# Kernel optimization log

Measured on AMD Instinct MI355X. Metric: run time of the kernel, lower is better.

## Reference

```python
import jax, jax.numpy as jnp
import numpy as np

M, K, N = 4096, 4096, 12288
GS = 128                 # quantization group size
G = K // GS              # number of groups
PACK = 8                 # int4 values per int32


def _pack_nibbles(key, shape_packed, axis_len):
    # generate random int4 values and pack 8 per int32 (bit-faithful GPTQ layout)
    nib = jax.random.randint(key, shape_packed[:1] + (PACK,) + shape_packed[1:], 0, 16, dtype=jnp.uint32)
    shifts = (jnp.arange(PACK, dtype=jnp.uint32) * 4)[None, :, None]
    return jnp.sum(nib << shifts, axis=1).astype(jnp.int32)


def setup_inputs() -> dict:
    key = jax.random.key(0)
    k1, k2, k3, k4, k5 = jax.random.split(key, 5)
    x = jax.random.normal(k1, (M, K), dtype=jnp.float32) * 0.05
    qweight = _pack_nibbles(k2, (K // PACK, N), K)          # [K/8, N] int32
    qzeros = _pack_nibbles(k3, (G, N // PACK), N)           # [G, N/8] int32
    scales = jax.random.uniform(k4, (G, N), dtype=jnp.float32, minval=0.001, maxval=0.01)
    bias = jax.random.normal(k5, (N,), dtype=jnp.float32) * 0.01
    return {"x": x, "qweight": qweight, "qzeros": qzeros, "scales": scales, "bias": bias}


def _unpack_rows(q):
    # [R, C] int32 -> [R*8, C] int4 values unpacked along rows
    shifts = (jnp.arange(PACK, dtype=jnp.uint32) * 4)[None, :, None]
    nib = (q.astype(jnp.uint32)[:, None, :] >> shifts) & jnp.uint32(0xF)
    return nib.reshape(q.shape[0] * PACK, q.shape[1])


def _unpack_cols(q):
    # [R, C] int32 -> [R, C*8] int4 values unpacked along columns
    shifts = (jnp.arange(PACK, dtype=jnp.uint32) * 4)[None, None, :]
    nib = (q.astype(jnp.uint32)[:, :, None] >> shifts) & jnp.uint32(0xF)
    return nib.reshape(q.shape[0], q.shape[1] * PACK)


def reference(x, qweight, qzeros, scales, bias):
    # dequantize: w[k,n] = (q[k,n] - (z[g,n]+1)) * s[g,n],  g = k // GS
    q = _unpack_rows(qweight).astype(jnp.float32)                    # [K, N]
    z = (_unpack_cols(qzeros).astype(jnp.float32) + 1.0)             # [G, N]
    s = scales                                                       # [G, N]
    w = (q.reshape(G, GS, N) - z[:, None, :]) * s[:, None, :]        # [G, GS, N]
    w = w.reshape(K, N)
    return x @ w + bias
```

## Files before the change

### kernel.cpp

```cpp
#include <hip/hip_runtime.h>
#include <hip/hip_bf16.h>

namespace {
constexpr int Md = 4096, Kd = 4096, Nd = 12288;
constexpr int BM = 256, BN = 128, BK = 64;
constexpr int TK = Kd / BK;
constexpr int THREADS = 256;
constexpr size_t A_BYTES = (size_t)Md * Kd * 2;
constexpr int AS_T = BM * BK;
constexpr int BS_T = BN * BK;
constexpr int LDS_BYTES = (2 * AS_T + BS_T) * 2;

typedef __attribute__((ext_vector_type(4))) float f4;
typedef __attribute__((ext_vector_type(8))) _Float16 h8;
typedef __attribute__((ext_vector_type(2))) _Float16 h2;

constexpr unsigned M4  = 0x000F000Fu;
constexpr unsigned MAG = 0x64006400u;

__device__ __forceinline__ unsigned pkrtz(float lo, float hi) {
  return __builtin_bit_cast(unsigned, __builtin_amdgcn_cvt_pkrtz(lo, hi));
}

__global__ __launch_bounds__(256)
void cvtA_perm(const float* __restrict__ X, unsigned short* __restrict__ Xb, int n8) {
  int i = blockIdx.x * blockDim.x + threadIdx.x;
  const int stride = gridDim.x * blockDim.x;
  for (; i < n8; i += stride) {
    const f4* p = (const f4*)X + (size_t)i * 2;
    f4 a = p[0], b = p[1];
    uint4 o;
    o.x = pkrtz(a[0], b[0]); o.y = pkrtz(a[1], b[1]);
    o.z = pkrtz(a[2], b[2]); o.w = pkrtz(a[3], b[3]);
    ((uint4*)Xb)[i] = o;
  }
}

template<bool AWS>
__global__ __launch_bounds__(THREADS, 2)
void qgemm7(const float* __restrict__ X, const unsigned short* __restrict__ Xb,
            const int* __restrict__ QW, const int* __restrict__ QZ,
            const float* __restrict__ SC, const float* __restrict__ BS,
            float* __restrict__ OUT)
{
  extern __shared__ char smem[];
  unsigned short* As = (unsigned short*)smem;
  unsigned short* Bs = (unsigned short*)(smem + 2 * AS_T * 2);

  const int nwg = gridDim.x, cpx = nwg >> 3, b = blockIdx.x;
  const int swz = (b & 7) * cpx + (b >> 3);
  const int bm = swz / (Nd / BN), bn = swz % (Nd / BN);
  const int m0 = bm * BM, n0 = bn * BN;

  const int tid = threadIdx.x, lane = tid & 63, wid = tid >> 6;
  const int wr = wid >> 1, wc = wid & 1;

  const int n_l = tid & 127;
  const int k8b = (tid >> 7) * 4;
  const int nab = n0 + n_l;

  f4 acc[8][4];
  #pragma unroll
  for (int i = 0; i < 8; ++i)
    #pragma unroll
    for (int j = 0; j < 4; ++j) acc[i][j] = {0.0f, 0.0f, 0.0f, 0.0f};

  auto stageA = [&](int t, int buf) {
    #pragma unroll
    for (int i = 0; i < 8; ++i) {
      const int c = i * THREADS + tid;
      const int r = c >> 3, kbl = c & 7;
      const unsigned short* src = Xb + (size_t)(m0 + r) * Kd + t * BK + ((kbl ^ (r & 7)) << 3);
      __builtin_amdgcn_global_load_lds(
          (const __attribute__((address_space(1))) unsigned*)src,
          (__attribute__((address_space(3))) unsigned*)(As + buf * AS_T + c * 8),
          16, 0, 0);
    }
  };
  auto stageA_f = [&](int t, int buf) {
    #pragma unroll
    for (int i = 0; i < 8; ++i) {
      const int c = i * THREADS + tid;
      const int r = c >> 3, kbl = c & 7;
      const f4* src = (const f4*)(X + (size_t)(m0 + r) * Kd + t * BK + ((kbl ^ (r & 7)) << 3));
      f4 a = src[0], bb = src[1];
      uint4 o;
      o.x = pkrtz(a[0], bb[0]); o.y = pkrtz(a[1], bb[1]);
      o.z = pkrtz(a[2], bb[2]); o.w = pkrtz(a[3], bb[3]);
      *(uint4*)(As + buf * AS_T + c * 8) = o;
    }
  };

  auto loadB = [&](int t, int* w, unsigned& hs2, unsigned& hz2) {
    const int* qp = QW + (size_t)(t * 8 + k8b) * Nd + nab;
    #pragma unroll
    for (int i = 0; i < 4; ++i) w[i] = qp[(size_t)i * Nd];
    const int g = t >> 1;
    const float s = SC[(size_t)g * Nd + nab];
    const int z32 = QZ[(size_t)g * (Nd / 8) + (nab >> 3)];
    const int z = (z32 >> ((nab & 7) * 4)) & 15;
    const unsigned hz = 0x6400u + (unsigned)z + 1u;
    hz2 = hz * 0x10001u;
    const unsigned short hs = __builtin_bit_cast(unsigned short, (_Float16)s);
    hs2 = (unsigned)hs * 0x10001u;
  };
  auto writeB = [&](const int* w, unsigned hs2, unsigned hz2) {
    const h2 vz = __builtin_bit_cast(h2, hz2);
    const h2 vs = __builtin_bit_cast(h2, hs2);
    #pragma unroll
    for (int i = 0; i < 4; ++i) {
      const unsigned q = (unsigned)w[i];
      const int k8 = k8b + i;
      const unsigned p0 = (q & M4) | MAG;
      const unsigned p1 = ((q >> 4) & M4) | MAG;
      const unsigned p2 = ((q >> 8) & M4) | MAG;
      const unsigned p3 = ((q >> 12) & M4) | MAG;
      const h2 f0 = (__builtin_bit_cast(h2, p0) - vz) * vs;
      const h2 f1 = (__builtin_bit_cast(h2, p1) - vz) * vs;
      const h2 f2 = (__builtin_bit_cast(h2, p2) - vz) * vs;
      const h2 f3 = (__builtin_bit_cast(h2, p3) - vz) * vs;
      uint4 o;
      o.x = __builtin_bit_cast(unsigned, f0);
      o.y = __builtin_bit_cast(unsigned, f1);
      o.z = __builtin_bit_cast(unsigned, f2);
      o.w = __builtin_bit_cast(unsigned, f3);
      *(uint4*)(Bs + n_l * BK + ((k8 ^ (n_l & 7)) << 3)) = o;
    }
  };

  auto mfma_tile = [&](int cb) {
    const unsigned short* Ab = As + cb * AS_T;
    #pragma unroll
    for (int ks = 0; ks < 2; ++ks) {
      h8 af[8], bf[4];
      const int kb = ks * 4 + (lane >> 4);
      #pragma unroll
      for (int mi = 0; mi < 8; ++mi) {
        const int r = wr * 128 + mi * 16 + (lane & 15);
        af[mi] = *(const h8*)&Ab[r * BK + ((kb ^ (r & 7)) << 3)];
      }
      #pragma unroll
      for (int ni = 0; ni < 4; ++ni) {
        const int cc = wc * 64 + ni * 16 + (lane & 15);
        bf[ni] = *(const h8*)&Bs[cc * BK + ((kb ^ (cc & 7)) << 3)];
      }
      #pragma unroll
      for (int mi = 0; mi < 8; ++mi)
        #pragma unroll
        for (int ni = 0; ni < 4; ++ni)
          acc[mi][ni] = __builtin_amdgcn_mfma_f32_16x16x32_f16(af[mi], bf[ni], acc[mi][ni], 0, 0, 0);
    }
  };

  int bw[4]; unsigned sHS, sHZ;
  int nbw[4]; unsigned nHS, nHZ;

  if constexpr (AWS) stageA(0, 0); else stageA_f(0, 0);
  loadB(0, bw, sHS, sHZ);
  writeB(bw, sHS, sHZ);
  __syncthreads();

  for (int t = 0; t < TK; ++t) {
    const int cb = t & 1;
    if (t + 1 < TK) {
      if constexpr (AWS) stageA(t + 1, cb ^ 1);
      loadB(t + 1, nbw, nHS, nHZ);
    }
    mfma_tile(cb);
    __syncthreads();
    if (t + 1 < TK) {
      if constexpr (!AWS) stageA_f(t + 1, cb ^ 1);
      writeB(nbw, nHS, nHZ);
    }
    __syncthreads();
  }

  #pragma unroll
  for (int ni = 0; ni < 4; ++ni) {
    const int gn = n0 + wc * 64 + ni * 16 + (lane & 15);
    const float bv = BS[gn];
    #pragma unroll
    for (int mi = 0; mi < 8; ++mi) {
      const int gm = m0 + wr * 128 + mi * 16 + ((lane >> 4) << 2);
      #pragma unroll
      for (int j = 0; j < 4; ++j)
        OUT[(size_t)(gm + j) * Nd + gn] = acc[mi][ni][j] + bv;
    }
  }
}
}

extern "C" void kernel_launch(void* const* d_in, const int* in_sizes, int n_in,
                              void* d_out, int out_size, void* d_ws, size_t ws_size,
                              hipStream_t stream) {
  const float* x  = (const float*)d_in[0];
  const int*   qw = (const int*)d_in[1];
  const int*   qz = (const int*)d_in[2];
  const float* sc = (const float*)d_in[3];
  const float* bs = (const float*)d_in[4];
  float* out = (float*)d_out;

  (void)hipFuncSetAttribute((const void*)qgemm7<true>,
                            hipFuncAttributeMaxDynamicSharedMemorySize, LDS_BYTES);
  (void)hipFuncSetAttribute((const void*)qgemm7<false>,
                            hipFuncAttributeMaxDynamicSharedMemorySize, LDS_BYTES);

  dim3 grid((Md / BM) * (Nd / BN));
  if (ws_size >= A_BYTES) {
    unsigned short* xh = (unsigned short*)d_ws;
    const int n8 = Md * Kd / 8;
    cvtA_perm<<<2048, 256, 0, stream>>>(x, xh, n8);
    qgemm7<true><<<grid, dim3(THREADS), LDS_BYTES, stream>>>(x, xh, qw, qz, sc, bs, out);
  } else {
    qgemm7<false><<<grid, dim3(THREADS), LDS_BYTES, stream>>>(x, nullptr, qw, qz, sc, bs, out);
  }
}
```

Before: 426.4 us.

## Enlarge tile to 256x256 with 8 waves and ping-pong interleaved LDS/MFMA schedule

The main kernel now uses 512 threads and a 256x256 output tile with double-buffered B in LDS. The main loop is unrolled by two K-steps and split into quarter MFMA phases with explicit barriers and raised priority, so LDS fragment reads, global A staging and B dequantisation interleave with the matrix ops. Tile reuse rises and load latency should be better hidden, at the cost of more LDS (128KB), more registers and hand-placed waitcnt and barrier ordering. The non-workspace fallback path is split out as a separate kernel that keeps the old 256x128 configuration.

Measured after the change: 401.3 us. -5.9%, faster.

```diff
diff --git a/kernel.cpp b/kernel.cpp
--- a/kernel.cpp
+++ b/kernel.cpp
@@ -3,13 +3,13 @@
 
 namespace {
 constexpr int Md = 4096, Kd = 4096, Nd = 12288;
-constexpr int BM = 256, BN = 128, BK = 64;
+constexpr int BM = 256, BN = 256, BK = 64;
 constexpr int TK = Kd / BK;
-constexpr int THREADS = 256;
+constexpr int THREADS = 512;
 constexpr size_t A_BYTES = (size_t)Md * Kd * 2;
 constexpr int AS_T = BM * BK;
 constexpr int BS_T = BN * BK;
-constexpr int LDS_BYTES = (2 * AS_T + BS_T) * 2;
+constexpr int LDS_BYTES = (2 * AS_T + 2 * BS_T) * 2;
 
 typedef __attribute__((ext_vector_type(4))) float f4;
 typedef __attribute__((ext_vector_type(8))) _Float16 h8;
@@ -17,6 +17,10 @@
 
 constexpr unsigned M4  = 0x000F000Fu;
 constexpr unsigned MAG = 0x64006400u;
+
+#define SBAR       asm volatile("s_barrier" ::: "memory")
+#define WAIT_LGKM0 asm volatile("s_waitcnt lgkmcnt(0)" ::: "memory")
+#define WAIT_VM0   asm volatile("s_waitcnt vmcnt(0)" ::: "memory")
 
 __device__ __forceinline__ unsigned pkrtz(float lo, float hi) {
   return __builtin_bit_cast(unsigned, __builtin_amdgcn_cvt_pkrtz(lo, hi));
@@ -36,9 +40,8 @@
   }
 }
 
-template<bool AWS>
 __global__ __launch_bounds__(THREADS, 2)
-void qgemm7(const float* __restrict__ X, const unsigned short* __restrict__ Xb,
+void qgemm8(const unsigned short* __restrict__ Xb,
             const int* __restrict__ QW, const int* __restrict__ QZ,
             const float* __restrict__ SC, const float* __restrict__ BS,
             float* __restrict__ OUT)
@@ -53,10 +56,11 @@
   const int m0 = bm * BM, n0 = bn * BN;
 
   const int tid = threadIdx.x, lane = tid & 63, wid = tid >> 6;
-  const int wr = wid >> 1, wc = wid & 1;
-
-  const int n_l = tid & 127;
-  const int k8b = (tid >> 7) * 4;
+  const int wr = wid >> 2, wc = wid & 3;
+  const int lr = lane & 15, lk = lane >> 4;
+
+  const int n_l = tid & 255;
+  const int k8b = (tid >> 8) * 4;
   const int nab = n0 + n_l;
 
   f4 acc[8][4];
@@ -65,9 +69,12 @@
     #pragma unroll
     for (int j = 0; j < 4; ++j) acc[i][j] = {0.0f, 0.0f, 0.0f, 0.0f};
 
-  auto stageA = [&](int t, int buf) {
-    #pragma unroll
-    for (int i = 0; i < 8; ++i) {
+  h8 afr[4][2];
+  h8 bfA[2][2], bfB[2][2];
+
+  auto stageA = [&](int t, int buf, int half) {
+    #pragma unroll
+    for (int i = half * 2; i < half * 2 + 2; ++i) {
       const int c = i * THREADS + tid;
       const int r = c >> 3, kbl = c & 7;
       const unsigned short* src = Xb + (size_t)(m0 + r) * Kd + t * BK + ((kbl ^ (r & 7)) << 3);
@@ -77,20 +84,185 @@
           16, 0, 0);
     }
   };
+  auto loadQW = [&](int t, int* w) {
+    const int* qp = QW + (size_t)(t * 8 + k8b) * Nd + nab;
+    #pragma unroll
+    for (int i = 0; i < 4; ++i) w[i] = qp[(size_t)i * Nd];
+  };
+  auto writeB = [&](const int* w, unsigned hs2, unsigned hz2, int buf) {
+    const h2 vz = __builtin_bit_cast(h2, hz2);
+    const h2 vs = __builtin_bit_cast(h2, hs2);
+    #pragma unroll
+    for (int i = 0; i < 4; ++i) {
+      const unsigned q = (unsigned)w[i];
+      const int k8 = k8b + i;
+      const unsigned p0 = (q & M4) | MAG;
+      const unsigned p1 = ((q >> 4) & M4) | MAG;
+      const unsigned p2 = ((q >> 8) & M4) | MAG;
+      const unsigned p3 = ((q >> 12) & M4) | MAG;
+      const h2 f0 = (__builtin_bit_cast(h2, p0) - vz) * vs;
+      const h2 f1 = (__builtin_bit_cast(h2, p1) - vz) * vs;
+      const h2 f2 = (__builtin_bit_cast(h2, p2) - vz) * vs;
+      const h2 f3 = (__builtin_bit_cast(h2, p3) - vz) * vs;
+      uint4 o;
+      o.x = __builtin_bit_cast(unsigned, f0);
+      o.y = __builtin_bit_cast(unsigned, f1);
+      o.z = __builtin_bit_cast(unsigned, f2);
+      o.w = __builtin_bit_cast(unsigned, f3);
+      *(uint4*)(Bs + buf * BS_T + n_l * BK + ((k8 ^ (n_l & 7)) << 3)) = o;
+    }
+  };
+  auto dsA = [&](int buf, int mih) {
+    const unsigned short* Ab = As + buf * AS_T;
+    #pragma unroll
+    for (int mi4 = 0; mi4 < 4; ++mi4) {
+      const int r = wr * 128 + (mih * 4 + mi4) * 16 + lr;
+      #pragma unroll
+      for (int ks = 0; ks < 2; ++ks) {
+        const int kb = ks * 4 + lk;
+        afr[mi4][ks] = *(const h8*)&Ab[r * BK + ((kb ^ (r & 7)) << 3)];
+      }
+    }
+  };
+  auto dsB = [&](int buf, int nih, h8 (&dst)[2][2]) {
+    const unsigned short* Bb = Bs + buf * BS_T;
+    #pragma unroll
+    for (int ni2 = 0; ni2 < 2; ++ni2) {
+      const int cc = wc * 64 + (nih * 2 + ni2) * 16 + lr;
+      #pragma unroll
+      for (int ks = 0; ks < 2; ++ks) {
+        const int kb = ks * 4 + lk;
+        dst[ni2][ks] = *(const h8*)&Bb[cc * BK + ((kb ^ (cc & 7)) << 3)];
+      }
+    }
+  };
+  auto mfmaQ = [&](int mih, int nih, h8 (&bfr)[2][2]) {
+    __builtin_amdgcn_s_setprio(1);
+    #pragma unroll
+    for (int mi4 = 0; mi4 < 4; ++mi4)
+      #pragma unroll
+      for (int ni2 = 0; ni2 < 2; ++ni2)
+        #pragma unroll
+        for (int ks = 0; ks < 2; ++ks)
+          acc[mih * 4 + mi4][nih * 2 + ni2] =
+            __builtin_amdgcn_mfma_f32_16x16x32_f16(afr[mi4][ks], bfr[ni2][ks],
+                                                   acc[mih * 4 + mi4][nih * 2 + ni2], 0, 0, 0);
+    __builtin_amdgcn_s_setprio(0);
+  };
+  auto makeH = [&](float s, int z32, unsigned& hs2, unsigned& hz2) {
+    const int z = (z32 >> ((nab & 7) * 4)) & 15;
+    hz2 = (0x6400u + (unsigned)z + 1u) * 0x10001u;
+    hs2 = (unsigned)__builtin_bit_cast(unsigned short, (_Float16)s) * 0x10001u;
+  };
+
+  int bw[4];
+  float sN; int zN;
+  unsigned hsC, hzC;
+
+  {
+    const float s0 = SC[(size_t)0 * Nd + nab];
+    const int z0 = QZ[(nab >> 3)];
+    loadQW(0, bw);
+    stageA(0, 0, 0); stageA(0, 0, 1);
+    makeH(s0, z0, hsC, hzC);
+    writeB(bw, hsC, hzC, 0);
+    WAIT_LGKM0; WAIT_VM0; SBAR;
+  }
+
+  for (int u = 0; u < TK / 2; ++u) {
+    const bool ns = (u < TK / 2 - 1);
+
+    dsA(0, 0); dsB(0, 0, bfA);
+    loadQW(2 * u + 1, bw);
+    stageA(2 * u + 1, 1, 0);
+    SBAR; mfmaQ(0, 0, bfA); SBAR;
+    dsB(0, 1, bfB);
+    stageA(2 * u + 1, 1, 1);
+    SBAR; mfmaQ(0, 1, bfB); SBAR;
+    dsA(0, 1);
+    SBAR; mfmaQ(1, 0, bfA); SBAR;
+    writeB(bw, hsC, hzC, 1);
+    mfmaQ(1, 1, bfB);
+    WAIT_LGKM0; WAIT_VM0; SBAR;
+
+    dsA(1, 0); dsB(1, 0, bfA);
+    if (ns) {
+      loadQW(2 * u + 2, bw);
+      sN = SC[(size_t)(u + 1) * Nd + nab];
+      zN = QZ[(size_t)(u + 1) * (Nd / 8) + (nab >> 3)];
+      stageA(2 * u + 2, 0, 0);
+    }
+    SBAR; mfmaQ(0, 0, bfA); SBAR;
+    dsB(1, 1, bfB);
+    if (ns) stageA(2 * u + 2, 0, 1);
+    SBAR; mfmaQ(0, 1, bfB); SBAR;
+    dsA(1, 1);
+    SBAR; mfmaQ(1, 0, bfA); SBAR;
+    if (ns) {
+      unsigned nhs, nhz;
+      makeH(sN, zN, nhs, nhz);
+      writeB(bw, nhs, nhz, 0);
+      hsC = nhs; hzC = nhz;
+    }
+    mfmaQ(1, 1, bfB);
+    WAIT_LGKM0; WAIT_VM0; SBAR;
+  }
+
+  #pragma unroll
+  for (int ni = 0; ni < 4; ++ni) {
+    const int gn = n0 + wc * 64 + ni * 16 + lr;
+    const float bv = BS[gn];
+    #pragma unroll
+    for (int mi = 0; mi < 8; ++mi) {
+      const int gm = m0 + wr * 128 + mi * 16 + (lk << 2);
+      #pragma unroll
+      for (int j = 0; j < 4; ++j)
+        OUT[(size_t)(gm + j) * Nd + gn] = acc[mi][ni][j] + bv;
+    }
+  }
+}
+
+__global__ __launch_bounds__(256, 2)
+void qgemm_fb(const float* __restrict__ X,
+              const int* __restrict__ QW, const int* __restrict__ QZ,
+              const float* __restrict__ SC, const float* __restrict__ BS,
+              float* __restrict__ OUT)
+{
+  constexpr int FBM = 256, FBN = 128;
+  constexpr int FAS = FBM * BK, FBS = FBN * BK;
+  extern __shared__ char smem[];
+  unsigned short* As = (unsigned short*)smem;
+  unsigned short* Bs = (unsigned short*)(smem + 2 * FAS * 2);
+
+  const int nwg = gridDim.x, cpx = nwg >> 3, b = blockIdx.x;
+  const int swz = (b & 7) * cpx + (b >> 3);
+  const int bm = swz / (Nd / FBN), bn = swz % (Nd / FBN);
+  const int m0 = bm * FBM, n0 = bn * FBN;
+  const int tid = threadIdx.x, lane = tid & 63, wid = tid >> 6;
+  const int wr = wid >> 1, wc = wid & 1;
+  const int n_l = tid & 127;
+  const int k8b = (tid >> 7) * 4;
+  const int nab = n0 + n_l;
+
+  f4 acc[8][4];
+  #pragma unroll
+  for (int i = 0; i < 8; ++i)
+    #pragma unroll
+    for (int j = 0; j < 4; ++j) acc[i][j] = {0.0f, 0.0f, 0.0f, 0.0f};
+
   auto stageA_f = [&](int t, int buf) {
     #pragma unroll
     for (int i = 0; i < 8; ++i) {
-      const int c = i * THREADS + tid;
+      const int c = i * 256 + tid;
       const int r = c >> 3, kbl = c & 7;
       const f4* src = (const f4*)(X + (size_t)(m0 + r) * Kd + t * BK + ((kbl ^ (r & 7)) << 3));
       f4 a = src[0], bb = src[1];
       uint4 o;
       o.x = pkrtz(a[0], bb[0]); o.y = pkrtz(a[1], bb[1]);
       o.z = pkrtz(a[2], bb[2]); o.w = pkrtz(a[3], bb[3]);
-      *(uint4*)(As + buf * AS_T + c * 8) = o;
-    }
-  };
-
+      *(uint4*)(As + buf * FAS + c * 8) = o;
+    }
+  };
   auto loadB = [&](int t, int* w, unsigned& hs2, unsigned& hz2) {
     const int* qp = QW + (size_t)(t * 8 + k8b) * Nd + nab;
     #pragma unroll
@@ -99,10 +271,8 @@
     const float s = SC[(size_t)g * Nd + nab];
     const int z32 = QZ[(size_t)g * (Nd / 8) + (nab >> 3)];
     const int z = (z32 >> ((nab & 7) * 4)) & 15;
-    const unsigned hz = 0x6400u + (unsigned)z + 1u;
-    hz2 = hz * 0x10001u;
-    const unsigned short hs = __builtin_bit_cast(unsigned short, (_Float16)s);
-    hs2 = (unsigned)hs * 0x10001u;
+    hz2 = (0x6400u + (unsigned)z + 1u) * 0x10001u;
+    hs2 = (unsigned)__builtin_bit_cast(unsigned short, (_Float16)s) * 0x10001u;
   };
   auto writeB = [&](const int* w, unsigned hs2, unsigned hz2) {
     const h2 vz = __builtin_bit_cast(h2, hz2);
@@ -127,9 +297,8 @@
       *(uint4*)(Bs + n_l * BK + ((k8 ^ (n_l & 7)) << 3)) = o;
     }
   };
-
   auto mfma_tile = [&](int cb) {
-    const unsigned short* Ab = As + cb * AS_T;
+    const unsigned short* Ab = As + cb * FAS;
     #pragma unroll
     for (int ks = 0; ks < 2; ++ks) {
       h8 af[8], bf[4];
@@ -154,27 +323,21 @@
 
   int bw[4]; unsigned sHS, sHZ;
   int nbw[4]; unsigned nHS, nHZ;
-
-  if constexpr (AWS) stageA(0, 0); else stageA_f(0, 0);
+  stageA_f(0, 0);
   loadB(0, bw, sHS, sHZ);
   writeB(bw, sHS, sHZ);
   __syncthreads();
-
   for (int t = 0; t < TK; ++t) {
     const int cb = t & 1;
-    if (t + 1 < TK) {
-      if constexpr (AWS) stageA(t + 1, cb ^ 1);
-      loadB(t + 1, nbw, nHS, nHZ);
-    }
+    if (t + 1 < TK) loadB(t + 1, nbw, nHS, nHZ);
     mfma_tile(cb);
     __syncthreads();
     if (t + 1 < TK) {
-      if constexpr (!AWS) stageA_f(t + 1, cb ^ 1);
+      stageA_f(t + 1, cb ^ 1);
       writeB(nbw, nHS, nHZ);
     }
     __syncthreads();
   }
-
   #pragma unroll
   for (int ni = 0; ni < 4; ++ni) {
     const int gn = n0 + wc * 64 + ni * 16 + (lane & 15);
@@ -200,18 +363,19 @@
   const float* bs = (const float*)d_in[4];
   float* out = (float*)d_out;
 
-  (void)hipFuncSetAttribute((const void*)qgemm7<true>,
+  (void)hipFuncSetAttribute((const void*)qgemm8,
                             hipFuncAttributeMaxDynamicSharedMemorySize, LDS_BYTES);
-  (void)hipFuncSetAttribute((const void*)qgemm7<false>,
-                            hipFuncAttributeMaxDynamicSharedMemorySize, LDS_BYTES);
-
-  dim3 grid((Md / BM) * (Nd / BN));
+  (void)hipFuncSetAttribute((const void*)qgemm_fb,
+                            hipFuncAttributeMaxDynamicSharedMemorySize, (2 * 256 * BK + 128 * BK) * 2);
+
   if (ws_size >= A_BYTES) {
     unsigned short* xh = (unsigned short*)d_ws;
     const int n8 = Md * Kd / 8;
     cvtA_perm<<<2048, 256, 0, stream>>>(x, xh, n8);
-    qgemm7<true><<<grid, dim3(THREADS), LDS_BYTES, stream>>>(x, xh, qw, qz, sc, bs, out);
+    dim3 grid((Md / BM) * (Nd / BN));
+    qgemm8<<<grid, dim3(THREADS), LDS_BYTES, stream>>>(xh, qw, qz, sc, bs, out);
   } else {
-    qgemm7<false><<<grid, dim3(THREADS), LDS_BYTES, stream>>>(x, nullptr, qw, qz, sc, bs, out);
-  }
-}
+    dim3 grid((Md / 256) * (Nd / 128));
+    qgemm_fb<<<grid, dim3(256), (2 * 256 * BK + 128 * BK) * 2, stream>>>(x, qw, qz, sc, bs, out);
+  }
+}
```
